# Kernel tuning notes

Hardware: AMD Instinct MI355X
Metric: run time of the kernel (lower is better)

The kernel has to match this reference:

```python
import jax, jax.numpy as jnp
import numpy as np

N, P, T, K = 20000, 5, 16, 3
IN, H, O = 150, 64, 128


def setup_inputs() -> dict:
    key = jax.random.key(0)
    k1, k2, k3, k4, k5 = jax.random.split(key, 5)
    x = jax.random.normal(k1, (N, IN), dtype=jnp.float32)
    conn_idx = jax.random.randint(k2, (N, P, T, K), 0, N, dtype=jnp.int32)
    conn_w = jax.random.uniform(k3, (N, P, T, K), dtype=jnp.float32)
    # learned params
    W1 = jax.random.normal(k4, (H, IN), dtype=jnp.float32) * 0.05   # linear_1 (no bias)
    Wg = jax.random.normal(k5, (O, H, P, T), dtype=jnp.float32) * 0.05  # geodesic conv weight
    bg = jnp.zeros((O,), dtype=jnp.float32)                          # geodesic conv bias
    return {"x": x, "conn_idx": conn_idx, "conn_w": conn_w, "W1": W1, "Wg": Wg, "bg": bg}


def reference(x, conn_idx, conn_w, W1, Wg, bg):
    # Linear + ReLU: [N, H]
    h = jax.nn.relu(x @ W1.T)
    # Geodesic patch gather: interpolate vertex features into P x T bins
    g = jnp.take(h, conn_idx, axis=0)                 # [N, P, T, K, H]
    patches = jnp.einsum('nptk,nptkh->npth', conn_w, g)  # [N, P, T, H]
    # Geodesic convolution: contract patch bins and channels
    out = jnp.einsum('npth,ohpt->no', patches, Wg) + bg  # [N, O]
    # L2 normalize per vertex
    norm = jnp.linalg.norm(out, axis=-1, keepdims=True)
    return out / norm
```

## Files before the change

kernel.cpp:

```cpp
#include <hip/hip_runtime.h>
#include <hip/hip_fp16.h>

#define NV   20000
#define KK   3
#define INF  150
#define HH   64
#define OO   128
#define PT   80
#define KTOT 5120
#define NB   80
#define RS   72
#define CB   (NB * RS)
#define XS   168
#define NBIN 40
#define CPS  41

typedef _Float16 fh8 __attribute__((ext_vector_type(8)));
typedef __attribute__((ext_vector_type(4))) float f32x4;
typedef __attribute__((ext_vector_type(8))) unsigned short u16x8;

__device__ __forceinline__ unsigned short f2h(float f) {
    return __half_as_ushort(__float2half(f));
}
__device__ __forceinline__ float h2f(unsigned short u) {
    return __half2float(__ushort_as_half(u));
}
__device__ __forceinline__ _Float16 u2h(unsigned short u) {
    union { unsigned short s; _Float16 h; } c; c.s = u; return c.h;
}

__global__ __launch_bounds__(256) void prep_kernel(
    const float* __restrict__ Wg, const float* __restrict__ x,
    const float* __restrict__ W1, unsigned short* __restrict__ W2,
    unsigned short* __restrict__ hb) {
    __shared__ __align__(16) unsigned char smem[32256];
    const int tid = threadIdx.x;

    if (blockIdx.x < 128) {
        float* lds = (float*)smem;
        const int o = blockIdx.x;
        const float* src = Wg + o * KTOT;
        for (int e = tid; e < KTOT / 4; e += 256) {
            const float4 v4 = ((const float4*)src)[e];
            const int t = e * 4;
            const int h = t / 80, bin = t - h * 80;
            lds[h * 81 + bin]     = v4.x;
            lds[h * 81 + bin + 1] = v4.y;
            lds[h * 81 + bin + 2] = v4.z;
            lds[h * 81 + bin + 3] = v4.w;
        }
        __syncthreads();
        for (int e = tid; e < KTOT / 2; e += 256) {
            const int t = e * 2;
            const unsigned int h0 = f2h(lds[(t & 63) * 81 + (t >> 6)]);
            const unsigned int h1 = f2h(lds[((t + 1) & 63) * 81 + ((t + 1) >> 6)]);
            *(unsigned int*)(W2 + (t >> 5) * 4096 + o * 32 + (t & 31)) =
                h0 | (h1 << 16);
        }
        return;
    }

    unsigned short* xs = (unsigned short*)smem;
    unsigned short* ws = xs + 32 * XS;
    const int n0 = (blockIdx.x - 128) * 32;

    {
        const float2* x2 = (const float2*)(x + (size_t)n0 * INF);
        for (int e = tid; e < 32 * (INF / 2); e += 256) {
            const int f = e * 2;
            const int r = f / INF, c = f - r * INF;
            const float2 v = x2[e];
            const unsigned int p =
                (unsigned int)f2h(v.x) | ((unsigned int)f2h(v.y) << 16);
            *(unsigned int*)(xs + r * XS + c) = p;
        }
    }
    for (int e = tid; e < 32 * 9; e += 256) {
        const int r = e / 9, c2 = e - r * 9;
        *(unsigned int*)(xs + r * XS + 150 + c2 * 2) = 0;
    }
    {
        const float2* w2p = (const float2*)W1;
        for (int e = tid; e < 64 * (INF / 2); e += 256) {
            const int f = e * 2;
            const int r = f / INF, c = f - r * INF;
            const float2 v = w2p[e];
            const unsigned int p =
                (unsigned int)f2h(v.x) | ((unsigned int)f2h(v.y) << 16);
            *(unsigned int*)(ws + r * XS + c) = p;
        }
    }
    for (int e = tid; e < 64 * 9; e += 256) {
        const int r = e / 9, c2 = e - r * 9;
        *(unsigned int*)(ws + r * XS + 150 + c2 * 2) = 0;
    }
    __syncthreads();

    const int wv   = tid >> 6;
    const int lane = tid & 63;
    const int q    = lane >> 4;
    const int r16  = lane & 15;
    const int o0   = wv * 16;

    f32x4 acc0 = {0.f, 0.f, 0.f, 0.f};
    f32x4 acc1 = acc0;
    #pragma unroll
    for (int s = 0; s < 5; s++) {
        const int kb = s * 32 + q * 8;
        fh8 a0 = *(const fh8*)(xs + r16 * XS + kb);
        fh8 a1 = *(const fh8*)(xs + (16 + r16) * XS + kb);
        fh8 b  = *(const fh8*)(ws + (o0 + r16) * XS + kb);
        acc0 = __builtin_amdgcn_mfma_f32_16x16x32_f16(a0, b, acc0, 0, 0, 0);
        acc1 = __builtin_amdgcn_mfma_f32_16x16x32_f16(a1, b, acc1, 0, 0, 0);
    }
    #pragma unroll
    for (int r = 0; r < 4; r++) {
        float v0 = acc0[r] > 0.f ? acc0[r] : 0.f;
        float v1 = acc1[r] > 0.f ? acc1[r] : 0.f;
        hb[(n0 + q * 4 + r) * HH + o0 + r16]      = f2h(v0);
        hb[(n0 + 16 + q * 4 + r) * HH + o0 + r16] = f2h(v1);
    }
}

__global__ __launch_bounds__(512, 2) void geo_kernel(
    const int*   __restrict__ conn_idx, const float* __restrict__ conn_w,
    const unsigned short* __restrict__ W2, const unsigned short* __restrict__ hb,
    float* __restrict__ out, unsigned short* __restrict__ parts) {
    __shared__ __align__(16) unsigned short pch[2 * CB];
    __shared__ __align__(16) unsigned short cp[NB * CPS * 8];

    const int tid  = threadIdx.x;
    const int ks   = blockIdx.x & 1;
    const int n0   = (blockIdx.x >> 1) * NB;
    const int wv   = tid >> 6;
    const int lane = tid & 63;
    const int q    = lane >> 4;
    const int r16  = lane & 15;
    const int j8   = tid & 7;
    const int v0   = tid >> 3;
    const bool lo  = (v0 < 16);
    const int bbase = ks * NBIN;
    const int Sbase = ks * (NBIN * 2);

    for (int e = tid; e < NB * NBIN; e += 512) {
        const int v = e / NBIN, cc = e - v * NBIN;
        const int g = (n0 + v) * (PT * KK) + (bbase + cc) * KK;
        u16x8 pk;
        pk[0] = (unsigned short)conn_idx[g];
        pk[1] = (unsigned short)conn_idx[g + 1];
        pk[2] = (unsigned short)conn_idx[g + 2];
        pk[3] = f2h(conn_w[g]);
        pk[4] = f2h(conn_w[g + 1]);
        pk[5] = f2h(conn_w[g + 2]);
        pk[6] = 0; pk[7] = 0;
        *(u16x8*)(cp + (v * CPS + cc) * 8) = pk;
    }

    f32x4 acc[5];
    #pragma unroll
    for (int m = 0; m < 5; m++) acc[m] = (f32x4){0.f, 0.f, 0.f, 0.f};

    u16x8 pa, pc;
    fh8   hva0, hva1, hva2, hvc0, hvc1, hvc2;

    auto loadg = [&](int cc) {
        pa = *(const u16x8*)(cp + (v0 * CPS + cc) * 8);
        hva0 = *(const fh8*)(hb + (int)pa[0] * HH + j8 * 8);
        hva1 = *(const fh8*)(hb + (int)pa[1] * HH + j8 * 8);
        hva2 = *(const fh8*)(hb + (int)pa[2] * HH + j8 * 8);
        if (lo) {
            pc = *(const u16x8*)(cp + ((v0 + 64) * CPS + cc) * 8);
            hvc0 = *(const fh8*)(hb + (int)pc[0] * HH + j8 * 8);
            hvc1 = *(const fh8*)(hb + (int)pc[1] * HH + j8 * 8);
            hvc2 = *(const fh8*)(hb + (int)pc[2] * HH + j8 * 8);
        }
    };
    auto cwr = [&](unsigned short* buf) {
        const _Float16 a0 = u2h(pa[3]), a1 = u2h(pa[4]), a2 = u2h(pa[5]);
        const fh8 A0 = {a0, a0, a0, a0, a0, a0, a0, a0};
        const fh8 A1 = {a1, a1, a1, a1, a1, a1, a1, a1};
        const fh8 A2 = {a2, a2, a2, a2, a2, a2, a2, a2};
        fh8 ra = hva0 * A0 + hva1 * A1 + hva2 * A2;
        *(fh8*)(buf + v0 * RS + j8 * 8) = ra;
        if (lo) {
            const _Float16 c0 = u2h(pc[3]), c1 = u2h(pc[4]), c2 = u2h(pc[5]);
            const fh8 C0 = {c0, c0, c0, c0, c0, c0, c0, c0};
            const fh8 C1 = {c1, c1, c1, c1, c1, c1, c1, c1};
            const fh8 C2 = {c2, c2, c2, c2, c2, c2, c2, c2};
            fh8 rc = hvc0 * C0 + hvc1 * C1 + hvc2 * C2;
            *(fh8*)(buf + (v0 + 64) * RS + j8 * 8) = rc;
        }
    };
    auto mfmaph = [&](const unsigned short* buf, int cc) {
        const unsigned short* wp =
            W2 + (Sbase + cc * 2) * 4096 + (wv * 16 + r16) * 32 + q * 8;
        const fh8 bf0 = *(const fh8*)(wp);
        const fh8 bf1 = *(const fh8*)(wp + 4096);
        #pragma unroll
        for (int s = 0; s < 2; s++) {
            const int ao = s * 32 + q * 8;
            const fh8 bf = s ? bf1 : bf0;
            #pragma unroll
            for (int m = 0; m < 5; m++) {
                fh8 af = *(const fh8*)(buf + (m * 16 + r16) * RS + ao);
                acc[m] = __builtin_amdgcn_mfma_f32_16x16x32_f16(af, bf, acc[m], 0, 0, 0);
            }
        }
    };

    __syncthreads();

    loadg(0);
    cwr(pch);
    __syncthreads();

    #pragma unroll 1
    for (int cc = 0; cc < NBIN; cc++) {
        if (cc + 1 < NBIN) loadg(cc + 1);
        mfmaph(&pch[(cc & 1) * CB], cc);
        if (cc + 1 < NBIN) cwr(&pch[((cc + 1) & 1) * CB]);
        __syncthreads();
    }

    if (ks == 0) {
        #pragma unroll
        for (int m = 0; m < 5; m++) {
            const int rb = n0 + m * 16 + q * 4;
            #pragma unroll
            for (int r = 0; r < 4; r++)
                out[(rb + r) * OO + wv * 16 + r16] = acc[m][r];
        }
    } else {
        #pragma unroll
        for (int m = 0; m < 5; m++) {
            const int rb = n0 + m * 16 + q * 4;
            #pragma unroll
            for (int r = 0; r < 4; r++)
                parts[(rb + r) * OO + wv * 16 + r16] = f2h(acc[m][r]);
        }
    }
}

__global__ __launch_bounds__(256) void norm_kernel(
    float* __restrict__ out, const unsigned short* __restrict__ parts,
    const float* __restrict__ bg) {
    const int tid  = threadIdx.x;
    const int n    = blockIdx.x * 32 + (tid >> 3);
    const int l    = tid & 7;
    const int base = n * OO + l * 16;

    float4 o4[4];
    #pragma unroll
    for (int i = 0; i < 4; i++)
        o4[i] = *(const float4*)(out + base + i * 4);

    u16x8 p0 = *(const u16x8*)(parts + base);
    u16x8 p1 = *(const u16x8*)(parts + base + 8);

    float4 b4[4];
    #pragma unroll
    for (int i = 0; i < 4; i++)
        b4[i] = *(const float4*)(bg + l * 16 + i * 4);

    float v[16];
    float s = 0.f;
    #pragma unroll
    for (int i = 0; i < 16; i++) {
        const float ov = (i & 3) == 0 ? o4[i >> 2].x :
                         (i & 3) == 1 ? o4[i >> 2].y :
                         (i & 3) == 2 ? o4[i >> 2].z : o4[i >> 2].w;
        const float bv = (i & 3) == 0 ? b4[i >> 2].x :
                         (i & 3) == 1 ? b4[i >> 2].y :
                         (i & 3) == 2 ? b4[i >> 2].z : b4[i >> 2].w;
        const float pv = h2f((i < 8) ? p0[i] : p1[i & 7]);
        v[i] = ov + pv + bv;
        s += v[i] * v[i];
    }
    for (int off = 4; off; off >>= 1) s += __shfl_down(s, off, 8);
    const float r = rsqrtf(__shfl(s, 0, 8));
    #pragma unroll
    for (int i = 0; i < 4; i++) {
        float4 w = {v[i * 4] * r, v[i * 4 + 1] * r,
                    v[i * 4 + 2] * r, v[i * 4 + 3] * r};
        *(float4*)(out + base + i * 4) = w;
    }
}

extern "C" void kernel_launch(void* const* d_in, const int* in_sizes, int n_in,
                              void* d_out, int out_size, void* d_ws, size_t ws_size,
                              hipStream_t stream) {
    const float* x        = (const float*)d_in[0];
    const int*   conn_idx = (const int*)  d_in[1];
    const float* conn_w   = (const float*)d_in[2];
    const float* W1       = (const float*)d_in[3];
    const float* Wg       = (const float*)d_in[4];
    const float* bg       = (const float*)d_in[5];
    float*       out      = (float*)d_out;

    unsigned short* W2    = (unsigned short*)d_ws;
    unsigned short* hb    = W2 + OO * KTOT;
    unsigned short* parts = hb + NV * HH;

    hipLaunchKernelGGL(prep_kernel, dim3(128 + NV / 32), dim3(256), 0, stream,
                       Wg, x, W1, W2, hb);
    hipLaunchKernelGGL(geo_kernel, dim3(2 * (NV / NB)), dim3(512), 0, stream,
                       conn_idx, conn_w, W2, hb, out, parts);
    hipLaunchKernelGGL(norm_kernel, dim3(NV / 32), dim3(256), 0, stream,
                       out, parts, bg);
}
```

Before: 158.6 us.

## Deepen geodesic gather pipeline to four LDS buffers with two bins per iteration

The geo kernel now processes two patch bins per loop iteration, using four LDS patch buffers and prefetching gathered vertex features two iterations ahead instead of one. This halves the number of barriers per bin and gives the random global gathers more time to complete. To make room in LDS, the packed connectivity table holds only half the bins. The second half is loaded into registers up front and written into LDS mid-loop. The extra live registers under a 512x2 launch bound risk spills or lower occupancy.

```diff
diff --git a/kernel.cpp b/kernel.cpp
--- a/kernel.cpp
+++ b/kernel.cpp
@@ -13,7 +13,8 @@
 #define CB   (NB * RS)
 #define XS   168
 #define NBIN 40
-#define CPS  41
+#define NCH  20
+#define CPS  21
 
 typedef _Float16 fh8 __attribute__((ext_vector_type(8)));
 typedef __attribute__((ext_vector_type(4))) float f32x4;
@@ -126,7 +127,7 @@
     const int*   __restrict__ conn_idx, const float* __restrict__ conn_w,
     const unsigned short* __restrict__ W2, const unsigned short* __restrict__ hb,
     float* __restrict__ out, unsigned short* __restrict__ parts) {
-    __shared__ __align__(16) unsigned short pch[2 * CB];
+    __shared__ __align__(16) unsigned short pch[4 * CB];
     __shared__ __align__(16) unsigned short cp[NB * CPS * 8];
 
     const int tid  = threadIdx.x;
@@ -142,8 +143,8 @@
     const int bbase = ks * NBIN;
     const int Sbase = ks * (NBIN * 2);
 
-    for (int e = tid; e < NB * NBIN; e += 512) {
-        const int v = e / NBIN, cc = e - v * NBIN;
+    for (int e = tid; e < NB * NCH; e += 512) {
+        const int v = e / NCH, cc = e - v * NCH;
         const int g = (n0 + v) * (PT * KK) + (bbase + cc) * KK;
         u16x8 pk;
         pk[0] = (unsigned short)conn_idx[g];
@@ -153,41 +154,67 @@
         pk[4] = f2h(conn_w[g + 1]);
         pk[5] = f2h(conn_w[g + 2]);
         pk[6] = 0; pk[7] = 0;
-        *(u16x8*)(cp + (v * CPS + cc) * 8) = pk;
+        *(u16x8*)(cp + (e + v) * 8) = pk;
+    }
+
+    u16x8 cpre0, cpre1, cpre2, cpre3 = {0, 0, 0, 0, 0, 0, 0, 0};
+    {
+        auto packc = [&](int e) {
+            const int v = e / NCH, cc = e - v * NCH;
+            const int g = (n0 + v) * (PT * KK) + (bbase + NCH + cc) * KK;
+            u16x8 pk;
+            pk[0] = (unsigned short)conn_idx[g];
+            pk[1] = (unsigned short)conn_idx[g + 1];
+            pk[2] = (unsigned short)conn_idx[g + 2];
+            pk[3] = f2h(conn_w[g]);
+            pk[4] = f2h(conn_w[g + 1]);
+            pk[5] = f2h(conn_w[g + 2]);
+            pk[6] = 0; pk[7] = 0;
+            return pk;
+        };
+        cpre0 = packc(tid);
+        cpre1 = packc(tid + 512);
+        cpre2 = packc(tid + 1024);
+        if (tid < NB * NCH - 1536) cpre3 = packc(tid + 1536);
     }
 
     f32x4 acc[5];
     #pragma unroll
     for (int m = 0; m < 5; m++) acc[m] = (f32x4){0.f, 0.f, 0.f, 0.f};
 
-    u16x8 pa, pc;
-    fh8   hva0, hva1, hva2, hvc0, hvc1, hvc2;
-
-    auto loadg = [&](int cc) {
-        pa = *(const u16x8*)(cp + (v0 * CPS + cc) * 8);
-        hva0 = *(const fh8*)(hb + (int)pa[0] * HH + j8 * 8);
-        hva1 = *(const fh8*)(hb + (int)pa[1] * HH + j8 * 8);
-        hva2 = *(const fh8*)(hb + (int)pa[2] * HH + j8 * 8);
+    u16x8 paA, pcA, paB, pcB;
+    fh8 hA0, hA1, hA2, gA0, gA1, gA2;
+    fh8 hB0, hB1, hB2, gB0, gB1, gB2;
+
+    auto loadg = [&](int cc, u16x8& pa, u16x8& pc,
+                     fh8& h0, fh8& h1, fh8& h2,
+                     fh8& g0, fh8& g1, fh8& g2) {
+        const int bb = (cc >= NCH) ? cc - NCH : cc;
+        pa = *(const u16x8*)(cp + (v0 * CPS + bb) * 8);
+        h0 = *(const fh8*)(hb + (int)pa[0] * HH + j8 * 8);
+        h1 = *(const fh8*)(hb + (int)pa[1] * HH + j8 * 8);
+        h2 = *(const fh8*)(hb + (int)pa[2] * HH + j8 * 8);
         if (lo) {
-            pc = *(const u16x8*)(cp + ((v0 + 64) * CPS + cc) * 8);
-            hvc0 = *(const fh8*)(hb + (int)pc[0] * HH + j8 * 8);
-            hvc1 = *(const fh8*)(hb + (int)pc[1] * HH + j8 * 8);
-            hvc2 = *(const fh8*)(hb + (int)pc[2] * HH + j8 * 8);
+            pc = *(const u16x8*)(cp + ((v0 + 64) * CPS + bb) * 8);
+            g0 = *(const fh8*)(hb + (int)pc[0] * HH + j8 * 8);
+            g1 = *(const fh8*)(hb + (int)pc[1] * HH + j8 * 8);
+            g2 = *(const fh8*)(hb + (int)pc[2] * HH + j8 * 8);
         }
     };
-    auto cwr = [&](unsigned short* buf) {
+    auto cwr = [&](unsigned short* buf, const u16x8& pa, const u16x8& pc,
+                   fh8 h0, fh8 h1, fh8 h2, fh8 g0, fh8 g1, fh8 g2) {
         const _Float16 a0 = u2h(pa[3]), a1 = u2h(pa[4]), a2 = u2h(pa[5]);
         const fh8 A0 = {a0, a0, a0, a0, a0, a0, a0, a0};
         const fh8 A1 = {a1, a1, a1, a1, a1, a1, a1, a1};
         const fh8 A2 = {a2, a2, a2, a2, a2, a2, a2, a2};
-        fh8 ra = hva0 * A0 + hva1 * A1 + hva2 * A2;
+        fh8 ra = h0 * A0 + h1 * A1 + h2 * A2;
         *(fh8*)(buf + v0 * RS + j8 * 8) = ra;
         if (lo) {
             const _Float16 c0 = u2h(pc[3]), c1 = u2h(pc[4]), c2 = u2h(pc[5]);
             const fh8 C0 = {c0, c0, c0, c0, c0, c0, c0, c0};
             const fh8 C1 = {c1, c1, c1, c1, c1, c1, c1, c1};
             const fh8 C2 = {c2, c2, c2, c2, c2, c2, c2, c2};
-            fh8 rc = hvc0 * C0 + hvc1 * C1 + hvc2 * C2;
+            fh8 rc = g0 * C0 + g1 * C1 + g2 * C2;
             *(fh8*)(buf + (v0 + 64) * RS + j8 * 8) = rc;
         }
     };
@@ -210,15 +237,41 @@
 
     __syncthreads();
 
-    loadg(0);
-    cwr(pch);
+    loadg(0, paA, pcA, hA0, hA1, hA2, gA0, gA1, gA2);
+    loadg(1, paB, pcB, hB0, hB1, hB2, gB0, gB1, gB2);
+    cwr(pch + 0 * CB, paA, pcA, hA0, hA1, hA2, gA0, gA1, gA2);
+    cwr(pch + 1 * CB, paB, pcB, hB0, hB1, hB2, gB0, gB1, gB2);
+    loadg(2, paA, pcA, hA0, hA1, hA2, gA0, gA1, gA2);
+    loadg(3, paB, pcB, hB0, hB1, hB2, gB0, gB1, gB2);
     __syncthreads();
 
     #pragma unroll 1
-    for (int cc = 0; cc < NBIN; cc++) {
-        if (cc + 1 < NBIN) loadg(cc + 1);
-        mfmaph(&pch[(cc & 1) * CB], cc);
-        if (cc + 1 < NBIN) cwr(&pch[((cc + 1) & 1) * CB]);
+    for (int p = 0; p < 20; p++) {
+        const int c0 = 2 * p;
+        if (p < 19) {
+            cwr(pch + ((c0 + 2) & 3) * CB, paA, pcA, hA0, hA1, hA2, gA0, gA1, gA2);
+            cwr(pch + ((c0 + 3) & 3) * CB, paB, pcB, hB0, hB1, hB2, gB0, gB1, gB2);
+        }
+        if (p == 8) {
+            *(u16x8*)(cp + (tid + tid / NCH) * 8) = cpre0;
+            {
+                const int e1 = tid + 512;
+                *(u16x8*)(cp + (e1 + e1 / NCH) * 8) = cpre1;
+                const int e2 = tid + 1024;
+                *(u16x8*)(cp + (e2 + e2 / NCH) * 8) = cpre2;
+            }
+            if (tid < NB * NCH - 1536) {
+                const int e3 = tid + 1536;
+                *(u16x8*)(cp + (e3 + e3 / NCH) * 8) = cpre3;
+            }
+            __syncthreads();
+        }
+        if (p < 18) {
+            loadg(c0 + 4, paA, pcA, hA0, hA1, hA2, gA0, gA1, gA2);
+            loadg(c0 + 5, paB, pcB, hB0, hB1, hB2, gB0, gB1, gB2);
+        }
+        mfmaph(pch + (c0 & 3) * CB, c0);
+        mfmaph(pch + ((c0 + 1) & 3) * CB, c0 + 1);
         __syncthreads();
     }
 
```

Result: slower. 193.1 us (+21.7%).

## Split geodesic K reduction four ways and chunk connection packing to cut LDS

Applied to the files above, without the earlier changes.

The split of the patch-bin reduction in geo_kernel grows from two ways to four, so 1000 blocks run instead of 500. Each block handles 20 bins, and the connectivity packing buffer is staged in two 10-bin chunks to shrink LDS use. The launch bound now allows 8 blocks per CU. The norm kernel sums three fp16 partial buffers instead of one. The trade is more fp16 partial traffic and rounding in exchange for higher occupancy and parallelism, and the workspace must be large enough for three partial arrays.

```diff
diff --git a/kernel.cpp b/kernel.cpp
--- a/kernel.cpp
+++ b/kernel.cpp
@@ -12,8 +12,9 @@
 #define RS   72
 #define CB   (NB * RS)
 #define XS   168
-#define NBIN 40
-#define CPS  41
+#define NBIN 20
+#define NCH  10
+#define CPS  11
 
 typedef _Float16 fh8 __attribute__((ext_vector_type(8)));
 typedef __attribute__((ext_vector_type(4))) float f32x4;
@@ -122,7 +123,7 @@
     }
 }
 
-__global__ __launch_bounds__(512, 2) void geo_kernel(
+__global__ __launch_bounds__(512, 8) void geo_kernel(
     const int*   __restrict__ conn_idx, const float* __restrict__ conn_w,
     const unsigned short* __restrict__ W2, const unsigned short* __restrict__ hb,
     float* __restrict__ out, unsigned short* __restrict__ parts) {
@@ -130,8 +131,8 @@
     __shared__ __align__(16) unsigned short cp[NB * CPS * 8];
 
     const int tid  = threadIdx.x;
-    const int ks   = blockIdx.x & 1;
-    const int n0   = (blockIdx.x >> 1) * NB;
+    const int ks   = blockIdx.x & 3;
+    const int n0   = (blockIdx.x >> 2) * NB;
     const int wv   = tid >> 6;
     const int lane = tid & 63;
     const int q    = lane >> 4;
@@ -142,19 +143,23 @@
     const int bbase = ks * NBIN;
     const int Sbase = ks * (NBIN * 2);
 
-    for (int e = tid; e < NB * NBIN; e += 512) {
-        const int v = e / NBIN, cc = e - v * NBIN;
-        const int g = (n0 + v) * (PT * KK) + (bbase + cc) * KK;
-        u16x8 pk;
-        pk[0] = (unsigned short)conn_idx[g];
-        pk[1] = (unsigned short)conn_idx[g + 1];
-        pk[2] = (unsigned short)conn_idx[g + 2];
-        pk[3] = f2h(conn_w[g]);
-        pk[4] = f2h(conn_w[g + 1]);
-        pk[5] = f2h(conn_w[g + 2]);
-        pk[6] = 0; pk[7] = 0;
-        *(u16x8*)(cp + (v * CPS + cc) * 8) = pk;
-    }
+    auto packchunk = [&](int c0) {
+        for (int e = tid; e < NB * NCH; e += 512) {
+            const int v = e / NCH, cc = e - v * NCH;
+            const int g = (n0 + v) * (PT * KK) + (bbase + c0 + cc) * KK;
+            u16x8 pk;
+            pk[0] = (unsigned short)conn_idx[g];
+            pk[1] = (unsigned short)conn_idx[g + 1];
+            pk[2] = (unsigned short)conn_idx[g + 2];
+            pk[3] = f2h(conn_w[g]);
+            pk[4] = f2h(conn_w[g + 1]);
+            pk[5] = f2h(conn_w[g + 2]);
+            pk[6] = 0; pk[7] = 0;
+            *(u16x8*)(cp + (v * CPS + cc) * 8) = pk;
+        }
+    };
+
+    packchunk(0);
 
     f32x4 acc[5];
     #pragma unroll
@@ -164,12 +169,13 @@
     fh8   hva0, hva1, hva2, hvc0, hvc1, hvc2;
 
     auto loadg = [&](int cc) {
-        pa = *(const u16x8*)(cp + (v0 * CPS + cc) * 8);
+        const int bb = (cc >= NCH) ? cc - NCH : cc;
+        pa = *(const u16x8*)(cp + (v0 * CPS + bb) * 8);
         hva0 = *(const fh8*)(hb + (int)pa[0] * HH + j8 * 8);
         hva1 = *(const fh8*)(hb + (int)pa[1] * HH + j8 * 8);
         hva2 = *(const fh8*)(hb + (int)pa[2] * HH + j8 * 8);
         if (lo) {
-            pc = *(const u16x8*)(cp + ((v0 + 64) * CPS + cc) * 8);
+            pc = *(const u16x8*)(cp + ((v0 + 64) * CPS + bb) * 8);
             hvc0 = *(const fh8*)(hb + (int)pc[0] * HH + j8 * 8);
             hvc1 = *(const fh8*)(hb + (int)pc[1] * HH + j8 * 8);
             hvc2 = *(const fh8*)(hb + (int)pc[2] * HH + j8 * 8);
@@ -216,6 +222,10 @@
 
     #pragma unroll 1
     for (int cc = 0; cc < NBIN; cc++) {
+        if (cc == NCH - 1) {
+            packchunk(NCH);
+            __syncthreads();
+        }
         if (cc + 1 < NBIN) loadg(cc + 1);
         mfmaph(&pch[(cc & 1) * CB], cc);
         if (cc + 1 < NBIN) cwr(&pch[((cc + 1) & 1) * CB]);
@@ -231,12 +241,13 @@
                 out[(rb + r) * OO + wv * 16 + r16] = acc[m][r];
         }
     } else {
+        unsigned short* pp = parts + (ks - 1) * (NV * OO);
         #pragma unroll
         for (int m = 0; m < 5; m++) {
             const int rb = n0 + m * 16 + q * 4;
             #pragma unroll
             for (int r = 0; r < 4; r++)
-                parts[(rb + r) * OO + wv * 16 + r16] = f2h(acc[m][r]);
+                pp[(rb + r) * OO + wv * 16 + r16] = f2h(acc[m][r]);
         }
     }
 }
@@ -254,8 +265,12 @@
     for (int i = 0; i < 4; i++)
         o4[i] = *(const float4*)(out + base + i * 4);
 
-    u16x8 p0 = *(const u16x8*)(parts + base);
-    u16x8 p1 = *(const u16x8*)(parts + base + 8);
+    u16x8 p[3][2];
+    #pragma unroll
+    for (int s = 0; s < 3; s++) {
+        p[s][0] = *(const u16x8*)(parts + s * (NV * OO) + base);
+        p[s][1] = *(const u16x8*)(parts + s * (NV * OO) + base + 8);
+    }
 
     float4 b4[4];
     #pragma unroll
@@ -272,8 +287,8 @@
         const float bv = (i & 3) == 0 ? b4[i >> 2].x :
                          (i & 3) == 1 ? b4[i >> 2].y :
                          (i & 3) == 2 ? b4[i >> 2].z : b4[i >> 2].w;
-        const float pv = h2f((i < 8) ? p0[i] : p1[i & 7]);
-        v[i] = ov + pv + bv;
+        v[i] = ov + h2f(p[0][i >> 3][i & 7]) + h2f(p[1][i >> 3][i & 7]) +
+               h2f(p[2][i >> 3][i & 7]) + bv;
         s += v[i] * v[i];
     }
     for (int off = 4; off; off >>= 1) s += __shfl_down(s, off, 8);
@@ -303,7 +318,7 @@
 
     hipLaunchKernelGGL(prep_kernel, dim3(128 + NV / 32), dim3(256), 0, stream,
                        Wg, x, W1, W2, hb);
-    hipLaunchKernelGGL(geo_kernel, dim3(2 * (NV / NB)), dim3(512), 0, stream,
+    hipLaunchKernelGGL(geo_kernel, dim3(4 * (NV / NB)), dim3(512), 0, stream,
                        conn_idx, conn_w, W2, hb, out, parts);
     hipLaunchKernelGGL(norm_kernel, dim3(NV / 32), dim3(256), 0, stream,
                        out, parts, bg);
```

After: 204.5 us. 28.9% more time.
